# Performance work log

Hardware: AMD Instinct MI355X
Metric: run time of the kernel (lower is better)

The kernel has to match this reference:

```python
import jax, jax.numpy as jnp
import numpy as np

B, NAG = 8192, 16          # scenes, agents per scene
CIN, CH = 64, 128          # gnn_in_channels, gnn_out_channels
R2 = 8.0 * 8.0             # comm_range squared
BOX = 20.0                 # positions sampled uniformly in [0, BOX]^2


def _lin(k, fi, fo):
    k1, k2 = jax.random.split(k)
    s = 1.0 / np.sqrt(fi)
    W = jax.random.uniform(k1, (fi, fo), jnp.float32, -s, s)
    b = jax.random.uniform(k2, (fo,), jnp.float32, -s, s)
    return W, b


def setup_inputs() -> dict:
    key = jax.random.key(0)
    ks = jax.random.split(key, 10)
    x = jax.random.normal(ks[0], (B * NAG, CIN), jnp.float32)          # VAE mu per agent
    pos = jax.random.uniform(ks[1], (B, NAG, 2), jnp.float32) * BOX    # sensor xy positions
    W_rel1, b_rel1 = _lin(ks[2], CIN, CH)
    W_root1, _ = _lin(ks[3], CIN, CH)
    W_rel2, b_rel2 = _lin(ks[4], CH, CH)
    W_root2, _ = _lin(ks[5], CH, CH)
    Wh1, bh1 = _lin(ks[6], 2 * CH, 64)
    Wh2, bh2 = _lin(ks[7], 64, 32)
    Wh3, bh3 = _lin(ks[8], 32, 16)
    return dict(x=x, pos=pos, W_rel1=W_rel1, b_rel1=b_rel1, W_root1=W_root1,
                W_rel2=W_rel2, b_rel2=b_rel2, W_root2=W_root2,
                Wh1=Wh1, bh1=bh1, Wh2=Wh2, bh2=bh2, Wh3=Wh3, bh3=bh3)


def _graph_conv(h, adj, W_rel, b_rel, W_root):
    # PyG GraphConv (aggr='add'): out_i = W_rel @ sum_{j in N(i)} h_j + b_rel + W_root @ h_i
    nb = adj.shape[0]
    hb = h.reshape(nb, NAG, h.shape[-1])                 # [B, n, C]
    agg = jnp.einsum('bij,bjc->bic', adj, hb)            # neighbor sum within each scene
    return agg.reshape(h.shape[0], -1) @ W_rel + b_rel + h @ W_root


def reference(x, pos, W_rel1, b_rel1, W_root1, W_rel2, b_rel2, W_root2,
              Wh1, bh1, Wh2, bh2, Wh3, bh3):
    # radius_graph (batch-isolated, loop=False) as a per-scene dense mask
    diff = pos[:, :, None, :] - pos[:, None, :, :]       # [B, n, n, 2]
    d2 = jnp.sum(diff * diff, axis=-1)                   # [B, n, n]
    eye = jnp.eye(NAG, dtype=bool)
    adj = ((d2 <= R2) & ~eye).astype(x.dtype)            # [B, n, n]
    # Dropout(p=0.2) omitted (eval / deterministic reference).
    x1 = jax.nn.relu(_graph_conv(x, adj, W_rel1, b_rel1, W_root1))   # named 'x1' (inplace ReLU)
    x2 = jax.nn.relu(_graph_conv(x1, adj, W_rel2, b_rel2, W_root2))  # named 'x2' (inplace ReLU)
    h = jnp.concatenate([x1, x2], axis=-1)               # JumpingKnowledge('cat')
    h = jax.nn.relu(h @ Wh1 + bh1)
    h = jax.nn.relu(h @ Wh2 + bh2)
    out = h @ Wh3 + bh3                                  # [N, 16]
    return out.reshape(B, NAG, 16)
```

## Files before the change

kernel.cpp:

```cpp
#include <hip/hip_runtime.h>

#define NSCENE 8192
#define NAG 16
#define R2f 64.0f

typedef unsigned short u16;
typedef __attribute__((ext_vector_type(8))) short short8;
typedef __attribute__((ext_vector_type(4))) float f32x4;

#define OFF_B1 0
#define OFF_B2 16384
#define OFF_H1 49152
#define OFF_H2 65536
#define OFF_H3 67584
#define SWZ_UNITS 8512

__device__ __forceinline__ u16 f2b(float f) {
    unsigned u = __float_as_uint(f);
    unsigned r = u + 0x7FFFu + ((u >> 16) & 1u);
    return (u16)(r >> 16);
}

__global__ __launch_bounds__(256) void swizzle_w(
    const float* __restrict__ Wrel1, const float* __restrict__ Wroot1,
    const float* __restrict__ Wrel2, const float* __restrict__ Wroot2,
    const float* __restrict__ Wh1,  const float* __restrict__ Wh2,
    const float* __restrict__ Wh3,  u16* __restrict__ ws)
{
    const int u = blockIdx.x * 256 + threadIdx.x;
    if (u >= SWZ_UNITS) return;

    int v, T, N, ksplit;
    const float *W, *W2;
    u16* dst;
    if (u < 2048)      { v = u;        T = 8; N = 128; ksplit = 64;  W = Wroot1; W2 = Wrel1; dst = ws + OFF_B1 + v * 8; }
    else if (u < 6144) { v = u - 2048; T = 8; N = 128; ksplit = 128; W = Wroot2; W2 = Wrel2; dst = ws + OFF_B2 + v * 8; }
    else if (u < 8192) { v = u - 6144; T = 4; N = 64;  ksplit = 1 << 30; W = Wh1; W2 = Wh1; dst = ws + OFF_H1 + v * 8; }
    else if (u < 8448) { v = u - 8192; T = 2; N = 32;  ksplit = 1 << 30; W = Wh2; W2 = Wh2; dst = ws + OFF_H2 + v * 8; }
    else               { v = u - 8448; T = 1; N = 16;  ksplit = 1 << 30; W = Wh3; W2 = Wh3; dst = ws + OFF_H3 + v * 8; }

    const int lane = v & 63;
    const int t = (v >> 6) % T;
    const int s = (v >> 6) / T;
    const int n = t * 16 + (lane & 15);
    const int k0 = s * 32 + (lane >> 4) * 8;
    #pragma unroll
    for (int j = 0; j < 8; ++j) {
        const int k = k0 + j;
        const float val = (k < ksplit) ? W[k * N + n] : W2[(k - ksplit) * N + n];
        dst[j] = f2b(val);
    }
}

__device__ __forceinline__ void unpack2(unsigned w, float& a, float& b) {
    a = __uint_as_float(w << 16);
    b = __uint_as_float(w & 0xFFFF0000u);
}

__global__ __launch_bounds__(256) void gnn_mfma(
    const float* __restrict__ x, const float* __restrict__ pos,
    const float* __restrict__ brel1, const float* __restrict__ brel2,
    const float* __restrict__ bh1,  const float* __restrict__ bh2,
    const float* __restrict__ bh3,
    const u16* __restrict__ ws, float* __restrict__ out)
{
    __shared__ __align__(16) u16 XA[16 * 136];
    __shared__ __align__(16) u16 X12[16 * 272];
    __shared__ __align__(16) u16 X2s[16 * 136];
    __shared__ __align__(16) u16 H1s[16 * 72];
    __shared__ __align__(16) u16 H2s[16 * 48];
    __shared__ unsigned mask[NAG];

    const int t = threadIdx.x;
    const int scene = blockIdx.x;
    const int wv = t >> 6;
    const int lane = t & 63;
    const int mrow = lane & 15;
    const int q = lane >> 4;

    {
        const int i0 = t * 4;
        const float4 v = *(const float4*)(x + scene * (NAG * 64) + i0);
        u16* d = &XA[(i0 >> 6) * 136 + (i0 & 63)];
        d[0] = f2b(v.x); d[1] = f2b(v.y); d[2] = f2b(v.z); d[3] = f2b(v.w);
    }
    if (t < NAG) {
        const float* pp = pos + scene * (NAG * 2);
        const float ax = pp[2 * t], ay = pp[2 * t + 1];
        unsigned m = 0;
        for (int j = 0; j < NAG; ++j) {
            const float dx = ax - pp[2 * j], dy = ay - pp[2 * j + 1];
            if (dx * dx + dy * dy <= R2f && j != t) m |= (1u << j);
        }
        mask[t] = m;
    }
    __syncthreads();

    {
        const int a = t >> 4, c0 = (t & 15) * 4;
        const unsigned m = mask[a];
        float s0 = 0.f, s1 = 0.f, s2 = 0.f, s3 = 0.f;
        for (int j = 0; j < NAG; ++j) {
            const unsigned* p = (const unsigned*)&XA[j * 136 + c0];
            float f0, f1, f2, f3;
            unpack2(p[0], f0, f1); unpack2(p[1], f2, f3);
            const bool on = (m >> j) & 1;
            s0 += on ? f0 : 0.f; s1 += on ? f1 : 0.f;
            s2 += on ? f2 : 0.f; s3 += on ? f3 : 0.f;
        }
        u16* d = &XA[a * 136 + 64 + c0];
        d[0] = f2b(s0); d[1] = f2b(s1); d[2] = f2b(s2); d[3] = f2b(s3);
    }
    __syncthreads();

    {
        const float bias0 = brel1[wv * 32 + mrow];
        const float bias1 = brel1[wv * 32 + 16 + mrow];
        f32x4 acc0 = {0.f, 0.f, 0.f, 0.f}, acc1 = acc0;
        #pragma unroll
        for (int s = 0; s < 4; ++s) {
            const short8 a = *(const short8*)&XA[mrow * 136 + s * 32 + q * 8];
            const short8 b0 = *(const short8*)&ws[OFF_B1 + ((s * 8 + 2 * wv) * 64 + lane) * 8];
            const short8 b1 = *(const short8*)&ws[OFF_B1 + ((s * 8 + 2 * wv + 1) * 64 + lane) * 8];
            acc0 = __builtin_amdgcn_mfma_f32_16x16x32_bf16(a, b0, acc0, 0, 0, 0);
            acc1 = __builtin_amdgcn_mfma_f32_16x16x32_bf16(a, b1, acc1, 0, 0, 0);
        }
        #pragma unroll
        for (int r = 0; r < 4; ++r) {
            const int row = q * 4 + r;
            float v0 = acc0[r] + bias0; v0 = v0 > 0.f ? v0 : 0.f;
            float v1 = acc1[r] + bias1; v1 = v1 > 0.f ? v1 : 0.f;
            X12[row * 272 + wv * 32 + mrow] = f2b(v0);
            X12[row * 272 + wv * 32 + 16 + mrow] = f2b(v1);
        }
    }
    __syncthreads();

    {
        const int a = t >> 4, c0 = (t & 15) * 8;
        const unsigned m = mask[a];
        float s0=0.f,s1=0.f,s2=0.f,s3=0.f,s4=0.f,s5=0.f,s6=0.f,s7=0.f;
        for (int j = 0; j < NAG; ++j) {
            const unsigned* p = (const unsigned*)&X12[j * 272 + c0];
            float f0,f1,f2,f3,f4,f5,f6,f7;
            unpack2(p[0], f0, f1); unpack2(p[1], f2, f3);
            unpack2(p[2], f4, f5); unpack2(p[3], f6, f7);
            const bool on = (m >> j) & 1;
            s0 += on ? f0 : 0.f; s1 += on ? f1 : 0.f; s2 += on ? f2 : 0.f; s3 += on ? f3 : 0.f;
            s4 += on ? f4 : 0.f; s5 += on ? f5 : 0.f; s6 += on ? f6 : 0.f; s7 += on ? f7 : 0.f;
        }
        u16* d = &X12[a * 272 + 128 + c0];
        d[0]=f2b(s0); d[1]=f2b(s1); d[2]=f2b(s2); d[3]=f2b(s3);
        d[4]=f2b(s4); d[5]=f2b(s5); d[6]=f2b(s6); d[7]=f2b(s7);
    }
    __syncthreads();

    {
        const float bias0 = brel2[wv * 32 + mrow];
        const float bias1 = brel2[wv * 32 + 16 + mrow];
        f32x4 acc0 = {0.f, 0.f, 0.f, 0.f}, acc1 = acc0;
        #pragma unroll
        for (int s = 0; s < 8; ++s) {
            const short8 a = *(const short8*)&X12[mrow * 272 + s * 32 + q * 8];
            const short8 b0 = *(const short8*)&ws[OFF_B2 + ((s * 8 + 2 * wv) * 64 + lane) * 8];
            const short8 b1 = *(const short8*)&ws[OFF_B2 + ((s * 8 + 2 * wv + 1) * 64 + lane) * 8];
            acc0 = __builtin_amdgcn_mfma_f32_16x16x32_bf16(a, b0, acc0, 0, 0, 0);
            acc1 = __builtin_amdgcn_mfma_f32_16x16x32_bf16(a, b1, acc1, 0, 0, 0);
        }
        #pragma unroll
        for (int r = 0; r < 4; ++r) {
            const int row = q * 4 + r;
            float v0 = acc0[r] + bias0; v0 = v0 > 0.f ? v0 : 0.f;
            float v1 = acc1[r] + bias1; v1 = v1 > 0.f ? v1 : 0.f;
            X2s[row * 136 + wv * 32 + mrow] = f2b(v0);
            X2s[row * 136 + wv * 32 + 16 + mrow] = f2b(v1);
        }
    }
    __syncthreads();

    {
        const float bias = bh1[wv * 16 + mrow];
        f32x4 acc = {0.f, 0.f, 0.f, 0.f};
        #pragma unroll
        for (int s = 0; s < 8; ++s) {
            const short8 a = (s < 4)
                ? *(const short8*)&X12[mrow * 272 + s * 32 + q * 8]
                : *(const short8*)&X2s[mrow * 136 + (s - 4) * 32 + q * 8];
            const short8 b = *(const short8*)&ws[OFF_H1 + ((s * 4 + wv) * 64 + lane) * 8];
            acc = __builtin_amdgcn_mfma_f32_16x16x32_bf16(a, b, acc, 0, 0, 0);
        }
        #pragma unroll
        for (int r = 0; r < 4; ++r) {
            float v = acc[r] + bias; v = v > 0.f ? v : 0.f;
            H1s[(q * 4 + r) * 72 + wv * 16 + mrow] = f2b(v);
        }
    }
    __syncthreads();

    if (wv < 2) {
        const float bias = bh2[wv * 16 + mrow];
        f32x4 acc = {0.f, 0.f, 0.f, 0.f};
        #pragma unroll
        for (int s = 0; s < 2; ++s) {
            const short8 a = *(const short8*)&H1s[mrow * 72 + s * 32 + q * 8];
            const short8 b = *(const short8*)&ws[OFF_H2 + ((s * 2 + wv) * 64 + lane) * 8];
            acc = __builtin_amdgcn_mfma_f32_16x16x32_bf16(a, b, acc, 0, 0, 0);
        }
        #pragma unroll
        for (int r = 0; r < 4; ++r) {
            float v = acc[r] + bias; v = v > 0.f ? v : 0.f;
            H2s[(q * 4 + r) * 48 + wv * 16 + mrow] = f2b(v);
        }
    }
    __syncthreads();

    if (wv == 0) {
        const float bias = bh3[mrow];
        f32x4 acc = {0.f, 0.f, 0.f, 0.f};
        const short8 a = *(const short8*)&H2s[mrow * 48 + q * 8];
        const short8 b = *(const short8*)&ws[OFF_H3 + lane * 8];
        acc = __builtin_amdgcn_mfma_f32_16x16x32_bf16(a, b, acc, 0, 0, 0);
        float* o = out + scene * (NAG * 16);
        #pragma unroll
        for (int r = 0; r < 4; ++r)
            o[(q * 4 + r) * 16 + mrow] = acc[r] + bias;
    }
}

extern "C" void kernel_launch(void* const* d_in, const int* in_sizes, int n_in,
                              void* d_out, int out_size, void* d_ws, size_t ws_size,
                              hipStream_t stream) {
    const float* x      = (const float*)d_in[0];
    const float* pos    = (const float*)d_in[1];
    const float* Wrel1  = (const float*)d_in[2];
    const float* brel1  = (const float*)d_in[3];
    const float* Wroot1 = (const float*)d_in[4];
    const float* Wrel2  = (const float*)d_in[5];
    const float* brel2  = (const float*)d_in[6];
    const float* Wroot2 = (const float*)d_in[7];
    const float* Wh1    = (const float*)d_in[8];
    const float* bh1    = (const float*)d_in[9];
    const float* Wh2    = (const float*)d_in[10];
    const float* bh2    = (const float*)d_in[11];
    const float* Wh3    = (const float*)d_in[12];
    const float* bh3    = (const float*)d_in[13];
    u16* ws = (u16*)d_ws;

    swizzle_w<<<(SWZ_UNITS + 255) / 256, 256, 0, stream>>>(
        Wrel1, Wroot1, Wrel2, Wroot2, Wh1, Wh2, Wh3, ws);
    gnn_mfma<<<NSCENE, 256, 0, stream>>>(
        x, pos, brel1, brel2, bh1, bh2, bh3, ws, (float*)d_out);
}
```

Before: 146.1 us.

## Fuse weight conversion into persistent kernel with register-resident weights and MFMA aggregation

After: 144.2 us. No clear change (-1.3%).

```diff
diff --git a/kernel.cpp b/kernel.cpp
--- a/kernel.cpp
+++ b/kernel.cpp
@@ -1,19 +1,15 @@
 #include <hip/hip_runtime.h>
 
-#define NSCENE 8192
 #define NAG 16
+#define SPB 16
+#define NBLK 512
 #define R2f 64.0f
 
 typedef unsigned short u16;
 typedef __attribute__((ext_vector_type(8))) short short8;
 typedef __attribute__((ext_vector_type(4))) float f32x4;
 
-#define OFF_B1 0
-#define OFF_B2 16384
-#define OFF_H1 49152
-#define OFF_H2 65536
-#define OFF_H3 67584
-#define SWZ_UNITS 8512
+#define MFMA(a, b, c) __builtin_amdgcn_mfma_f32_16x16x32_bf16(a, b, c, 0, 0, 0)
 
 __device__ __forceinline__ u16 f2b(float f) {
     unsigned u = __float_as_uint(f);
@@ -21,209 +17,220 @@
     return (u16)(r >> 16);
 }
 
-__global__ __launch_bounds__(256) void swizzle_w(
-    const float* __restrict__ Wrel1, const float* __restrict__ Wroot1,
-    const float* __restrict__ Wrel2, const float* __restrict__ Wroot2,
-    const float* __restrict__ Wh1,  const float* __restrict__ Wh2,
-    const float* __restrict__ Wh3,  u16* __restrict__ ws)
+__device__ __forceinline__ short8 load_wfrag(const float* __restrict__ W, int N,
+                                             int tile, int s, int q, int mrow) {
+    const float* p = W + (size_t)(s * 32 + q * 8) * N + tile * 16 + mrow;
+    union { short8 v; unsigned u[4]; } r;
+    #pragma unroll
+    for (int jj = 0; jj < 4; ++jj) {
+        const float f0 = p[(2 * jj) * N];
+        const float f1 = p[(2 * jj + 1) * N];
+        r.u[jj] = (unsigned)f2b(f0) | ((unsigned)f2b(f1) << 16);
+    }
+    return r.v;
+}
+
+__device__ __forceinline__ short8 make_adjB(unsigned m, int q) {
+    union { short8 v; unsigned u[4]; } r;
+    #pragma unroll
+    for (int jj = 0; jj < 4; ++jj) {
+        const int k0 = q * 8 + 2 * jj;
+        const unsigned lo = ((m >> k0) & 1u) ? 0x3F80u : 0u;
+        const unsigned hi = ((m >> (k0 + 1)) & 1u) ? 0x3F80u : 0u;
+        r.u[jj] = lo | (hi << 16);
+    }
+    return r.v;
+}
+
+__device__ __forceinline__ void relu_store4(u16* d, f32x4 a) {
+    const unsigned p0 = (unsigned)f2b(fmaxf(a[0], 0.f)) | ((unsigned)f2b(fmaxf(a[1], 0.f)) << 16);
+    const unsigned p1 = (unsigned)f2b(fmaxf(a[2], 0.f)) | ((unsigned)f2b(fmaxf(a[3], 0.f)) << 16);
+    uint2 u; u.x = p0; u.y = p1;
+    *(uint2*)d = u;
+}
+
+__global__ __launch_bounds__(256, 2) void gnn_fused2(
+    const float* __restrict__ x, const float* __restrict__ pos,
+    const float* __restrict__ Wrel1, const float* __restrict__ brel1,
+    const float* __restrict__ Wroot1,
+    const float* __restrict__ Wrel2, const float* __restrict__ brel2,
+    const float* __restrict__ Wroot2,
+    const float* __restrict__ Wh1, const float* __restrict__ bh1,
+    const float* __restrict__ Wh2, const float* __restrict__ bh2,
+    const float* __restrict__ Wh3, const float* __restrict__ bh3,
+    float* __restrict__ out)
 {
-    const int u = blockIdx.x * 256 + threadIdx.x;
-    if (u >= SWZ_UNITS) return;
-
-    int v, T, N, ksplit;
-    const float *W, *W2;
-    u16* dst;
-    if (u < 2048)      { v = u;        T = 8; N = 128; ksplit = 64;  W = Wroot1; W2 = Wrel1; dst = ws + OFF_B1 + v * 8; }
-    else if (u < 6144) { v = u - 2048; T = 8; N = 128; ksplit = 128; W = Wroot2; W2 = Wrel2; dst = ws + OFF_B2 + v * 8; }
-    else if (u < 8192) { v = u - 6144; T = 4; N = 64;  ksplit = 1 << 30; W = Wh1; W2 = Wh1; dst = ws + OFF_H1 + v * 8; }
-    else if (u < 8448) { v = u - 8192; T = 2; N = 32;  ksplit = 1 << 30; W = Wh2; W2 = Wh2; dst = ws + OFF_H2 + v * 8; }
-    else               { v = u - 8448; T = 1; N = 16;  ksplit = 1 << 30; W = Wh3; W2 = Wh3; dst = ws + OFF_H3 + v * 8; }
-
-    const int lane = v & 63;
-    const int t = (v >> 6) % T;
-    const int s = (v >> 6) / T;
-    const int n = t * 16 + (lane & 15);
-    const int k0 = s * 32 + (lane >> 4) * 8;
-    #pragma unroll
-    for (int j = 0; j < 8; ++j) {
-        const int k = k0 + j;
-        const float val = (k < ksplit) ? W[k * N + n] : W2[(k - ksplit) * N + n];
-        dst[j] = f2b(val);
-    }
-}
-
-__device__ __forceinline__ void unpack2(unsigned w, float& a, float& b) {
-    a = __uint_as_float(w << 16);
-    b = __uint_as_float(w & 0xFFFF0000u);
-}
-
-__global__ __launch_bounds__(256) void gnn_mfma(
-    const float* __restrict__ x, const float* __restrict__ pos,
-    const float* __restrict__ brel1, const float* __restrict__ brel2,
-    const float* __restrict__ bh1,  const float* __restrict__ bh2,
-    const float* __restrict__ bh3,
-    const u16* __restrict__ ws, float* __restrict__ out)
-{
-    __shared__ __align__(16) u16 XA[16 * 136];
-    __shared__ __align__(16) u16 X12[16 * 272];
-    __shared__ __align__(16) u16 X2s[16 * 136];
-    __shared__ __align__(16) u16 H1s[16 * 72];
-    __shared__ __align__(16) u16 H2s[16 * 48];
+    __shared__ __align__(16) u16 xb[16 * 72];
+    __shared__ __align__(16) u16 yT[128 * 40];
+    __shared__ __align__(16) u16 x1b[16 * 136];
+    __shared__ __align__(16) u16 x2b[16 * 136];
+    __shared__ __align__(16) u16 h1b[16 * 72];
+    __shared__ __align__(16) u16 h2b[16 * 40];
     __shared__ unsigned mask[NAG];
 
     const int t = threadIdx.x;
-    const int scene = blockIdx.x;
     const int wv = t >> 6;
     const int lane = t & 63;
     const int mrow = lane & 15;
     const int q = lane >> 4;
-
-    {
-        const int i0 = t * 4;
-        const float4 v = *(const float4*)(x + scene * (NAG * 64) + i0);
-        u16* d = &XA[(i0 >> 6) * 136 + (i0 & 63)];
-        d[0] = f2b(v.x); d[1] = f2b(v.y); d[2] = f2b(v.z); d[3] = f2b(v.w);
-    }
-    if (t < NAG) {
-        const float* pp = pos + scene * (NAG * 2);
-        const float ax = pp[2 * t], ay = pp[2 * t + 1];
-        unsigned m = 0;
-        for (int j = 0; j < NAG; ++j) {
-            const float dx = ax - pp[2 * j], dy = ay - pp[2 * j + 1];
-            if (dx * dx + dy * dy <= R2f && j != t) m |= (1u << j);
-        }
-        mask[t] = m;
-    }
-    __syncthreads();
-
-    {
-        const int a = t >> 4, c0 = (t & 15) * 4;
-        const unsigned m = mask[a];
-        float s0 = 0.f, s1 = 0.f, s2 = 0.f, s3 = 0.f;
-        for (int j = 0; j < NAG; ++j) {
-            const unsigned* p = (const unsigned*)&XA[j * 136 + c0];
-            float f0, f1, f2, f3;
-            unpack2(p[0], f0, f1); unpack2(p[1], f2, f3);
-            const bool on = (m >> j) & 1;
-            s0 += on ? f0 : 0.f; s1 += on ? f1 : 0.f;
-            s2 += on ? f2 : 0.f; s3 += on ? f3 : 0.f;
-        }
-        u16* d = &XA[a * 136 + 64 + c0];
-        d[0] = f2b(s0); d[1] = f2b(s1); d[2] = f2b(s2); d[3] = f2b(s3);
-    }
-    __syncthreads();
-
-    {
-        const float bias0 = brel1[wv * 32 + mrow];
-        const float bias1 = brel1[wv * 32 + 16 + mrow];
-        f32x4 acc0 = {0.f, 0.f, 0.f, 0.f}, acc1 = acc0;
+    const int t0 = 2 * wv, t1 = 2 * wv + 1;
+
+    for (int i = t; i < 128 * 16; i += 256)
+        yT[(i >> 4) * 40 + 16 + (i & 15)] = 0;
+
+    short8 wr1[2][2], wo1[2][2], wr2[2][4], wo2[2][4], wh1f[8], wh2f[2], wh3f;
+    #pragma unroll
+    for (int i = 0; i < 2; ++i) {
+        #pragma unroll
+        for (int s = 0; s < 2; ++s) {
+            wr1[i][s] = load_wfrag(Wrel1, 128, t0 + i, s, q, mrow);
+            wo1[i][s] = load_wfrag(Wroot1, 128, t0 + i, s, q, mrow);
+        }
         #pragma unroll
         for (int s = 0; s < 4; ++s) {
-            const short8 a = *(const short8*)&XA[mrow * 136 + s * 32 + q * 8];
-            const short8 b0 = *(const short8*)&ws[OFF_B1 + ((s * 8 + 2 * wv) * 64 + lane) * 8];
-            const short8 b1 = *(const short8*)&ws[OFF_B1 + ((s * 8 + 2 * wv + 1) * 64 + lane) * 8];
-            acc0 = __builtin_amdgcn_mfma_f32_16x16x32_bf16(a, b0, acc0, 0, 0, 0);
-            acc1 = __builtin_amdgcn_mfma_f32_16x16x32_bf16(a, b1, acc1, 0, 0, 0);
-        }
-        #pragma unroll
-        for (int r = 0; r < 4; ++r) {
-            const int row = q * 4 + r;
-            float v0 = acc0[r] + bias0; v0 = v0 > 0.f ? v0 : 0.f;
-            float v1 = acc1[r] + bias1; v1 = v1 > 0.f ? v1 : 0.f;
-            X12[row * 272 + wv * 32 + mrow] = f2b(v0);
-            X12[row * 272 + wv * 32 + 16 + mrow] = f2b(v1);
-        }
-    }
-    __syncthreads();
-
-    {
-        const int a = t >> 4, c0 = (t & 15) * 8;
-        const unsigned m = mask[a];
-        float s0=0.f,s1=0.f,s2=0.f,s3=0.f,s4=0.f,s5=0.f,s6=0.f,s7=0.f;
-        for (int j = 0; j < NAG; ++j) {
-            const unsigned* p = (const unsigned*)&X12[j * 272 + c0];
-            float f0,f1,f2,f3,f4,f5,f6,f7;
-            unpack2(p[0], f0, f1); unpack2(p[1], f2, f3);
-            unpack2(p[2], f4, f5); unpack2(p[3], f6, f7);
-            const bool on = (m >> j) & 1;
-            s0 += on ? f0 : 0.f; s1 += on ? f1 : 0.f; s2 += on ? f2 : 0.f; s3 += on ? f3 : 0.f;
-            s4 += on ? f4 : 0.f; s5 += on ? f5 : 0.f; s6 += on ? f6 : 0.f; s7 += on ? f7 : 0.f;
-        }
-        u16* d = &X12[a * 272 + 128 + c0];
-        d[0]=f2b(s0); d[1]=f2b(s1); d[2]=f2b(s2); d[3]=f2b(s3);
-        d[4]=f2b(s4); d[5]=f2b(s5); d[6]=f2b(s6); d[7]=f2b(s7);
-    }
-    __syncthreads();
-
-    {
-        const float bias0 = brel2[wv * 32 + mrow];
-        const float bias1 = brel2[wv * 32 + 16 + mrow];
-        f32x4 acc0 = {0.f, 0.f, 0.f, 0.f}, acc1 = acc0;
-        #pragma unroll
-        for (int s = 0; s < 8; ++s) {
-            const short8 a = *(const short8*)&X12[mrow * 272 + s * 32 + q * 8];
-            const short8 b0 = *(const short8*)&ws[OFF_B2 + ((s * 8 + 2 * wv) * 64 + lane) * 8];
-            const short8 b1 = *(const short8*)&ws[OFF_B2 + ((s * 8 + 2 * wv + 1) * 64 + lane) * 8];
-            acc0 = __builtin_amdgcn_mfma_f32_16x16x32_bf16(a, b0, acc0, 0, 0, 0);
-            acc1 = __builtin_amdgcn_mfma_f32_16x16x32_bf16(a, b1, acc1, 0, 0, 0);
-        }
-        #pragma unroll
-        for (int r = 0; r < 4; ++r) {
-            const int row = q * 4 + r;
-            float v0 = acc0[r] + bias0; v0 = v0 > 0.f ? v0 : 0.f;
-            float v1 = acc1[r] + bias1; v1 = v1 > 0.f ? v1 : 0.f;
-            X2s[row * 136 + wv * 32 + mrow] = f2b(v0);
-            X2s[row * 136 + wv * 32 + 16 + mrow] = f2b(v1);
-        }
-    }
-    __syncthreads();
-
-    {
-        const float bias = bh1[wv * 16 + mrow];
-        f32x4 acc = {0.f, 0.f, 0.f, 0.f};
-        #pragma unroll
-        for (int s = 0; s < 8; ++s) {
-            const short8 a = (s < 4)
-                ? *(const short8*)&X12[mrow * 272 + s * 32 + q * 8]
-                : *(const short8*)&X2s[mrow * 136 + (s - 4) * 32 + q * 8];
-            const short8 b = *(const short8*)&ws[OFF_H1 + ((s * 4 + wv) * 64 + lane) * 8];
-            acc = __builtin_amdgcn_mfma_f32_16x16x32_bf16(a, b, acc, 0, 0, 0);
-        }
-        #pragma unroll
-        for (int r = 0; r < 4; ++r) {
-            float v = acc[r] + bias; v = v > 0.f ? v : 0.f;
-            H1s[(q * 4 + r) * 72 + wv * 16 + mrow] = f2b(v);
-        }
-    }
-    __syncthreads();
-
-    if (wv < 2) {
-        const float bias = bh2[wv * 16 + mrow];
-        f32x4 acc = {0.f, 0.f, 0.f, 0.f};
-        #pragma unroll
-        for (int s = 0; s < 2; ++s) {
-            const short8 a = *(const short8*)&H1s[mrow * 72 + s * 32 + q * 8];
-            const short8 b = *(const short8*)&ws[OFF_H2 + ((s * 2 + wv) * 64 + lane) * 8];
-            acc = __builtin_amdgcn_mfma_f32_16x16x32_bf16(a, b, acc, 0, 0, 0);
-        }
-        #pragma unroll
-        for (int r = 0; r < 4; ++r) {
-            float v = acc[r] + bias; v = v > 0.f ? v : 0.f;
-            H2s[(q * 4 + r) * 48 + wv * 16 + mrow] = f2b(v);
-        }
-    }
-    __syncthreads();
-
-    if (wv == 0) {
-        const float bias = bh3[mrow];
-        f32x4 acc = {0.f, 0.f, 0.f, 0.f};
-        const short8 a = *(const short8*)&H2s[mrow * 48 + q * 8];
-        const short8 b = *(const short8*)&ws[OFF_H3 + lane * 8];
-        acc = __builtin_amdgcn_mfma_f32_16x16x32_bf16(a, b, acc, 0, 0, 0);
-        float* o = out + scene * (NAG * 16);
-        #pragma unroll
-        for (int r = 0; r < 4; ++r)
-            o[(q * 4 + r) * 16 + mrow] = acc[r] + bias;
+            wr2[i][s] = load_wfrag(Wrel2, 128, t0 + i, s, q, mrow);
+            wo2[i][s] = load_wfrag(Wroot2, 128, t0 + i, s, q, mrow);
+        }
+    }
+    #pragma unroll
+    for (int s = 0; s < 8; ++s) wh1f[s] = load_wfrag(Wh1, 64, wv, s, q, mrow);
+    #pragma unroll
+    for (int s = 0; s < 2; ++s) wh2f[s] = load_wfrag(Wh2, 32, wv & 1, s, q, mrow);
+    wh3f = load_wfrag(Wh3, 16, 0, 0, q, mrow);
+
+    const float4 br1a = *(const float4*)(brel1 + t0 * 16 + q * 4);
+    const float4 br1b = *(const float4*)(brel1 + t1 * 16 + q * 4);
+    const float4 br2a = *(const float4*)(brel2 + t0 * 16 + q * 4);
+    const float4 br2b = *(const float4*)(brel2 + t1 * 16 + q * 4);
+    const float4 bb1  = *(const float4*)(bh1 + wv * 16 + q * 4);
+    const float4 bb2  = *(const float4*)(bh2 + (wv & 1) * 16 + q * 4);
+    const float4 bb3  = *(const float4*)(bh3 + q * 4);
+
+    #pragma unroll 1
+    for (int g = 0; g < SPB; ++g) {
+        const size_t scene = (size_t)blockIdx.x * SPB + g;
+
+        {
+            const int i0 = t * 4;
+            const float4 v = *(const float4*)(x + scene * (NAG * 64) + i0);
+            const unsigned p0 = (unsigned)f2b(v.x) | ((unsigned)f2b(v.y) << 16);
+            const unsigned p1 = (unsigned)f2b(v.z) | ((unsigned)f2b(v.w) << 16);
+            uint2 u; u.x = p0; u.y = p1;
+            *(uint2*)&xb[(i0 >> 6) * 72 + (i0 & 63)] = u;
+        }
+        if (t < NAG) {
+            const float* pp = pos + scene * (NAG * 2);
+            const float ax = pp[2 * t], ay = pp[2 * t + 1];
+            unsigned m = 0;
+            for (int j = 0; j < NAG; ++j) {
+                const float dx = ax - pp[2 * j], dy = ay - pp[2 * j + 1];
+                if (dx * dx + dy * dy <= R2f && j != t) m |= (1u << j);
+            }
+            mask[t] = m;
+        }
+        __syncthreads();
+
+        const short8 adjB = make_adjB(mask[mrow], q);
+
+        {
+            f32x4 a0 = {0.f, 0.f, 0.f, 0.f}, a1 = a0;
+            #pragma unroll
+            for (int s = 0; s < 2; ++s) {
+                const short8 b = *(const short8*)&xb[mrow * 72 + s * 32 + q * 8];
+                a0 = MFMA(wr1[0][s], b, a0);
+                a1 = MFMA(wr1[1][s], b, a1);
+            }
+            #pragma unroll
+            for (int r = 0; r < 4; ++r) {
+                yT[(t0 * 16 + q * 4 + r) * 40 + mrow] = f2b(a0[r]);
+                yT[(t1 * 16 + q * 4 + r) * 40 + mrow] = f2b(a1[r]);
+            }
+        }
+        __syncthreads();
+
+        {
+            f32x4 a0 = {br1a.x, br1a.y, br1a.z, br1a.w};
+            f32x4 a1 = {br1b.x, br1b.y, br1b.z, br1b.w};
+            const short8 ya0 = *(const short8*)&yT[(t0 * 16 + mrow) * 40 + q * 8];
+            const short8 ya1 = *(const short8*)&yT[(t1 * 16 + mrow) * 40 + q * 8];
+            a0 = MFMA(ya0, adjB, a0);
+            a1 = MFMA(ya1, adjB, a1);
+            #pragma unroll
+            for (int s = 0; s < 2; ++s) {
+                const short8 b = *(const short8*)&xb[mrow * 72 + s * 32 + q * 8];
+                a0 = MFMA(wo1[0][s], b, a0);
+                a1 = MFMA(wo1[1][s], b, a1);
+            }
+            relu_store4(&x1b[mrow * 136 + t0 * 16 + q * 4], a0);
+            relu_store4(&x1b[mrow * 136 + t1 * 16 + q * 4], a1);
+        }
+        __syncthreads();
+
+        {
+            f32x4 a0 = {0.f, 0.f, 0.f, 0.f}, a1 = a0;
+            #pragma unroll
+            for (int s = 0; s < 4; ++s) {
+                const short8 b = *(const short8*)&x1b[mrow * 136 + s * 32 + q * 8];
+                a0 = MFMA(wr2[0][s], b, a0);
+                a1 = MFMA(wr2[1][s], b, a1);
+            }
+            #pragma unroll
+            for (int r = 0; r < 4; ++r) {
+                yT[(t0 * 16 + q * 4 + r) * 40 + mrow] = f2b(a0[r]);
+                yT[(t1 * 16 + q * 4 + r) * 40 + mrow] = f2b(a1[r]);
+            }
+        }
+        __syncthreads();
+
+        {
+            f32x4 a0 = {br2a.x, br2a.y, br2a.z, br2a.w};
+            f32x4 a1 = {br2b.x, br2b.y, br2b.z, br2b.w};
+            const short8 ya0 = *(const short8*)&yT[(t0 * 16 + mrow) * 40 + q * 8];
+            const short8 ya1 = *(const short8*)&yT[(t1 * 16 + mrow) * 40 + q * 8];
+            a0 = MFMA(ya0, adjB, a0);
+            a1 = MFMA(ya1, adjB, a1);
+            #pragma unroll
+            for (int s = 0; s < 4; ++s) {
+                const short8 b = *(const short8*)&x1b[mrow * 136 + s * 32 + q * 8];
+                a0 = MFMA(wo2[0][s], b, a0);
+                a1 = MFMA(wo2[1][s], b, a1);
+            }
+            relu_store4(&x2b[mrow * 136 + t0 * 16 + q * 4], a0);
+            relu_store4(&x2b[mrow * 136 + t1 * 16 + q * 4], a1);
+        }
+        __syncthreads();
+
+        {
+            f32x4 a = {bb1.x, bb1.y, bb1.z, bb1.w};
+            #pragma unroll
+            for (int s = 0; s < 8; ++s) {
+                const short8 b = (s < 4)
+                    ? *(const short8*)&x1b[mrow * 136 + s * 32 + q * 8]
+                    : *(const short8*)&x2b[mrow * 136 + (s - 4) * 32 + q * 8];
+                a = MFMA(wh1f[s], b, a);
+            }
+            relu_store4(&h1b[mrow * 72 + wv * 16 + q * 4], a);
+        }
+        __syncthreads();
+
+        if (wv < 2) {
+            f32x4 a = {bb2.x, bb2.y, bb2.z, bb2.w};
+            #pragma unroll
+            for (int s = 0; s < 2; ++s) {
+                const short8 b = *(const short8*)&h1b[mrow * 72 + s * 32 + q * 8];
+                a = MFMA(wh2f[s], b, a);
+            }
+            relu_store4(&h2b[mrow * 40 + wv * 16 + q * 4], a);
+        }
+        __syncthreads();
+
+        if (wv == 0) {
+            f32x4 a = {bb3.x, bb3.y, bb3.z, bb3.w};
+            const short8 b = *(const short8*)&h2b[mrow * 40 + q * 8];
+            a = MFMA(wh3f, b, a);
+            float4 o; o.x = a[0]; o.y = a[1]; o.z = a[2]; o.w = a[3];
+            *(float4*)(out + scene * (NAG * 16) + mrow * 16 + q * 4) = o;
+        }
     }
 }
 
@@ -244,10 +251,8 @@
     const float* bh2    = (const float*)d_in[11];
     const float* Wh3    = (const float*)d_in[12];
     const float* bh3    = (const float*)d_in[13];
-    u16* ws = (u16*)d_ws;
-
-    swizzle_w<<<(SWZ_UNITS + 255) / 256, 256, 0, stream>>>(
-        Wrel1, Wroot1, Wrel2, Wroot2, Wh1, Wh2, Wh3, ws);
-    gnn_mfma<<<NSCENE, 256, 0, stream>>>(
-        x, pos, brel1, brel2, bh1, bh2, bh3, ws, (float*)d_out);
-}
+
+    gnn_fused2<<<NBLK, 256, 0, stream>>>(
+        x, pos, Wrel1, brel1, Wroot1, Wrel2, brel2, Wroot2,
+        Wh1, bh1, Wh2, bh2, Wh3, bh3, (float*)d_out);
+}
```

## Batch two scenes per pass, 4 per block, and do neighbor aggregation via MFMA

Applied to the files above, without the earlier changes.

New measurement: 166.4 us. +13.9%, slower.

```diff
diff --git a/kernel.cpp b/kernel.cpp
--- a/kernel.cpp
+++ b/kernel.cpp
@@ -1,12 +1,15 @@
 #include <hip/hip_runtime.h>
 
-#define NSCENE 8192
 #define NAG 16
+#define SPB 4
+#define NBLK 2048
 #define R2f 64.0f
 
 typedef unsigned short u16;
 typedef __attribute__((ext_vector_type(8))) short short8;
 typedef __attribute__((ext_vector_type(4))) float f32x4;
+
+#define MFMA(a, b, c) __builtin_amdgcn_mfma_f32_16x16x32_bf16(a, b, c, 0, 0, 0)
 
 #define OFF_B1 0
 #define OFF_B2 16384
@@ -52,178 +55,228 @@
     }
 }
 
-__device__ __forceinline__ void unpack2(unsigned w, float& a, float& b) {
-    a = __uint_as_float(w << 16);
-    b = __uint_as_float(w & 0xFFFF0000u);
-}
-
-__global__ __launch_bounds__(256) void gnn_mfma(
+__device__ __forceinline__ short8 ldfrag(const u16* __restrict__ ws, int off,
+                                         int T, int s, int tile, int lane) {
+    return *(const short8*)(ws + off + (size_t)(((s * T + tile) * 64 + lane) * 8));
+}
+
+__device__ __forceinline__ short8 make_adjB(unsigned m, int q) {
+    union { short8 v; unsigned u[4]; } r;
+    #pragma unroll
+    for (int jj = 0; jj < 4; ++jj) {
+        const int k0 = q * 8 + 2 * jj;
+        const unsigned lo = ((m >> k0) & 1u) ? 0x3F80u : 0u;
+        const unsigned hi = ((m >> (k0 + 1)) & 1u) ? 0x3F80u : 0u;
+        r.u[jj] = lo | (hi << 16);
+    }
+    return r.v;
+}
+
+__device__ __forceinline__ void relu_store4(u16* d, f32x4 a) {
+    const unsigned p0 = (unsigned)f2b(fmaxf(a[0], 0.f)) | ((unsigned)f2b(fmaxf(a[1], 0.f)) << 16);
+    const unsigned p1 = (unsigned)f2b(fmaxf(a[2], 0.f)) | ((unsigned)f2b(fmaxf(a[3], 0.f)) << 16);
+    uint2 u; u.x = p0; u.y = p1;
+    *(uint2*)d = u;
+}
+
+__global__ __launch_bounds__(256) void gnn_fused3(
     const float* __restrict__ x, const float* __restrict__ pos,
     const float* __restrict__ brel1, const float* __restrict__ brel2,
     const float* __restrict__ bh1,  const float* __restrict__ bh2,
     const float* __restrict__ bh3,
     const u16* __restrict__ ws, float* __restrict__ out)
 {
-    __shared__ __align__(16) u16 XA[16 * 136];
-    __shared__ __align__(16) u16 X12[16 * 272];
-    __shared__ __align__(16) u16 X2s[16 * 136];
-    __shared__ __align__(16) u16 H1s[16 * 72];
-    __shared__ __align__(16) u16 H2s[16 * 48];
-    __shared__ unsigned mask[NAG];
+    __shared__ __align__(16) u16 xb[2][16 * 72];
+    __shared__ __align__(16) u16 yT[2][128 * 40];
+    __shared__ __align__(16) u16 x1b[2][16 * 136];
+    __shared__ __align__(16) u16 x2b[2][16 * 136];
+    __shared__ __align__(16) u16 h1b[2][16 * 72];
+    __shared__ __align__(16) u16 h2b[2][16 * 40];
+    __shared__ unsigned mask[2][NAG];
 
     const int t = threadIdx.x;
-    const int scene = blockIdx.x;
-    const int wv = t >> 6;
-    const int lane = t & 63;
-    const int mrow = lane & 15;
-    const int q = lane >> 4;
-
-    {
-        const int i0 = t * 4;
-        const float4 v = *(const float4*)(x + scene * (NAG * 64) + i0);
-        u16* d = &XA[(i0 >> 6) * 136 + (i0 & 63)];
-        d[0] = f2b(v.x); d[1] = f2b(v.y); d[2] = f2b(v.z); d[3] = f2b(v.w);
+    const int wv = t >> 6, lane = t & 63, mrow = lane & 15, q = lane >> 4;
+    const int t0 = 2 * wv, t1 = 2 * wv + 1;
+
+    for (int i = t; i < 2 * 128 * 16; i += 256) {
+        const int slot = i >> 11, rem = i & 2047;
+        yT[slot][(rem >> 4) * 40 + 16 + (rem & 15)] = 0;
     }
-    if (t < NAG) {
-        const float* pp = pos + scene * (NAG * 2);
-        const float ax = pp[2 * t], ay = pp[2 * t + 1];
-        unsigned m = 0;
-        for (int j = 0; j < NAG; ++j) {
-            const float dx = ax - pp[2 * j], dy = ay - pp[2 * j + 1];
-            if (dx * dx + dy * dy <= R2f && j != t) m |= (1u << j);
-        }
-        mask[t] = m;
-    }
-    __syncthreads();
-
-    {
-        const int a = t >> 4, c0 = (t & 15) * 4;
-        const unsigned m = mask[a];
-        float s0 = 0.f, s1 = 0.f, s2 = 0.f, s3 = 0.f;
-        for (int j = 0; j < NAG; ++j) {
-            const unsigned* p = (const unsigned*)&XA[j * 136 + c0];
-            float f0, f1, f2, f3;
-            unpack2(p[0], f0, f1); unpack2(p[1], f2, f3);
-            const bool on = (m >> j) & 1;
-            s0 += on ? f0 : 0.f; s1 += on ? f1 : 0.f;
-            s2 += on ? f2 : 0.f; s3 += on ? f3 : 0.f;
-        }
-        u16* d = &XA[a * 136 + 64 + c0];
-        d[0] = f2b(s0); d[1] = f2b(s1); d[2] = f2b(s2); d[3] = f2b(s3);
-    }
-    __syncthreads();
-
-    {
-        const float bias0 = brel1[wv * 32 + mrow];
-        const float bias1 = brel1[wv * 32 + 16 + mrow];
-        f32x4 acc0 = {0.f, 0.f, 0.f, 0.f}, acc1 = acc0;
-        #pragma unroll
-        for (int s = 0; s < 4; ++s) {
-            const short8 a = *(const short8*)&XA[mrow * 136 + s * 32 + q * 8];
-            const short8 b0 = *(const short8*)&ws[OFF_B1 + ((s * 8 + 2 * wv) * 64 + lane) * 8];
-            const short8 b1 = *(const short8*)&ws[OFF_B1 + ((s * 8 + 2 * wv + 1) * 64 + lane) * 8];
-            acc0 = __builtin_amdgcn_mfma_f32_16x16x32_bf16(a, b0, acc0, 0, 0, 0);
-            acc1 = __builtin_amdgcn_mfma_f32_16x16x32_bf16(a, b1, acc1, 0, 0, 0);
-        }
-        #pragma unroll
-        for (int r = 0; r < 4; ++r) {
-            const int row = q * 4 + r;
-            float v0 = acc0[r] + bias0; v0 = v0 > 0.f ? v0 : 0.f;
-            float v1 = acc1[r] + bias1; v1 = v1 > 0.f ? v1 : 0.f;
-            X12[row * 272 + wv * 32 + mrow] = f2b(v0);
-            X12[row * 272 + wv * 32 + 16 + mrow] = f2b(v1);
-        }
-    }
-    __syncthreads();
-
-    {
-        const int a = t >> 4, c0 = (t & 15) * 8;
-        const unsigned m = mask[a];
-        float s0=0.f,s1=0.f,s2=0.f,s3=0.f,s4=0.f,s5=0.f,s6=0.f,s7=0.f;
-        for (int j = 0; j < NAG; ++j) {
-            const unsigned* p = (const unsigned*)&X12[j * 272 + c0];
-            float f0,f1,f2,f3,f4,f5,f6,f7;
-            unpack2(p[0], f0, f1); unpack2(p[1], f2, f3);
-            unpack2(p[2], f4, f5); unpack2(p[3], f6, f7);
-            const bool on = (m >> j) & 1;
-            s0 += on ? f0 : 0.f; s1 += on ? f1 : 0.f; s2 += on ? f2 : 0.f; s3 += on ? f3 : 0.f;
-            s4 += on ? f4 : 0.f; s5 += on ? f5 : 0.f; s6 += on ? f6 : 0.f; s7 += on ? f7 : 0.f;
-        }
-        u16* d = &X12[a * 272 + 128 + c0];
-        d[0]=f2b(s0); d[1]=f2b(s1); d[2]=f2b(s2); d[3]=f2b(s3);
-        d[4]=f2b(s4); d[5]=f2b(s5); d[6]=f2b(s6); d[7]=f2b(s7);
-    }
-    __syncthreads();
-
-    {
-        const float bias0 = brel2[wv * 32 + mrow];
-        const float bias1 = brel2[wv * 32 + 16 + mrow];
-        f32x4 acc0 = {0.f, 0.f, 0.f, 0.f}, acc1 = acc0;
-        #pragma unroll
-        for (int s = 0; s < 8; ++s) {
-            const short8 a = *(const short8*)&X12[mrow * 272 + s * 32 + q * 8];
-            const short8 b0 = *(const short8*)&ws[OFF_B2 + ((s * 8 + 2 * wv) * 64 + lane) * 8];
-            const short8 b1 = *(const short8*)&ws[OFF_B2 + ((s * 8 + 2 * wv + 1) * 64 + lane) * 8];
-            acc0 = __builtin_amdgcn_mfma_f32_16x16x32_bf16(a, b0, acc0, 0, 0, 0);
-            acc1 = __builtin_amdgcn_mfma_f32_16x16x32_bf16(a, b1, acc1, 0, 0, 0);
-        }
-        #pragma unroll
-        for (int r = 0; r < 4; ++r) {
-            const int row = q * 4 + r;
-            float v0 = acc0[r] + bias0; v0 = v0 > 0.f ? v0 : 0.f;
-            float v1 = acc1[r] + bias1; v1 = v1 > 0.f ? v1 : 0.f;
-            X2s[row * 136 + wv * 32 + mrow] = f2b(v0);
-            X2s[row * 136 + wv * 32 + 16 + mrow] = f2b(v1);
-        }
-    }
-    __syncthreads();
-
-    {
-        const float bias = bh1[wv * 16 + mrow];
-        f32x4 acc = {0.f, 0.f, 0.f, 0.f};
-        #pragma unroll
-        for (int s = 0; s < 8; ++s) {
-            const short8 a = (s < 4)
-                ? *(const short8*)&X12[mrow * 272 + s * 32 + q * 8]
-                : *(const short8*)&X2s[mrow * 136 + (s - 4) * 32 + q * 8];
-            const short8 b = *(const short8*)&ws[OFF_H1 + ((s * 4 + wv) * 64 + lane) * 8];
-            acc = __builtin_amdgcn_mfma_f32_16x16x32_bf16(a, b, acc, 0, 0, 0);
-        }
-        #pragma unroll
-        for (int r = 0; r < 4; ++r) {
-            float v = acc[r] + bias; v = v > 0.f ? v : 0.f;
-            H1s[(q * 4 + r) * 72 + wv * 16 + mrow] = f2b(v);
-        }
-    }
-    __syncthreads();
-
-    if (wv < 2) {
-        const float bias = bh2[wv * 16 + mrow];
-        f32x4 acc = {0.f, 0.f, 0.f, 0.f};
-        #pragma unroll
-        for (int s = 0; s < 2; ++s) {
-            const short8 a = *(const short8*)&H1s[mrow * 72 + s * 32 + q * 8];
-            const short8 b = *(const short8*)&ws[OFF_H2 + ((s * 2 + wv) * 64 + lane) * 8];
-            acc = __builtin_amdgcn_mfma_f32_16x16x32_bf16(a, b, acc, 0, 0, 0);
-        }
-        #pragma unroll
-        for (int r = 0; r < 4; ++r) {
-            float v = acc[r] + bias; v = v > 0.f ? v : 0.f;
-            H2s[(q * 4 + r) * 48 + wv * 16 + mrow] = f2b(v);
-        }
-    }
-    __syncthreads();
-
-    if (wv == 0) {
-        const float bias = bh3[mrow];
-        f32x4 acc = {0.f, 0.f, 0.f, 0.f};
-        const short8 a = *(const short8*)&H2s[mrow * 48 + q * 8];
-        const short8 b = *(const short8*)&ws[OFF_H3 + lane * 8];
-        acc = __builtin_amdgcn_mfma_f32_16x16x32_bf16(a, b, acc, 0, 0, 0);
-        float* o = out + scene * (NAG * 16);
-        #pragma unroll
-        for (int r = 0; r < 4; ++r)
-            o[(q * 4 + r) * 16 + mrow] = acc[r] + bias;
+
+    const float4 br1a = *(const float4*)(brel1 + t0 * 16 + q * 4);
+    const float4 br1b = *(const float4*)(brel1 + t1 * 16 + q * 4);
+    const float4 br2a = *(const float4*)(brel2 + t0 * 16 + q * 4);
+    const float4 br2b = *(const float4*)(brel2 + t1 * 16 + q * 4);
+    const float4 bb1  = *(const float4*)(bh1 + wv * 16 + q * 4);
+    const float4 bb2  = *(const float4*)(bh2 + (wv & 1) * 16 + q * 4);
+    const float4 bb3  = *(const float4*)(bh3 + q * 4);
+
+    #pragma unroll 1
+    for (int g = 0; g < SPB / 2; ++g) {
+        const size_t sA = (size_t)blockIdx.x * SPB + 2 * g;
+
+        {
+            const int i0 = t * 4;
+            #pragma unroll
+            for (int sl = 0; sl < 2; ++sl) {
+                const float4 v = *(const float4*)(x + (sA + sl) * (NAG * 64) + i0);
+                const unsigned p0 = (unsigned)f2b(v.x) | ((unsigned)f2b(v.y) << 16);
+                const unsigned p1 = (unsigned)f2b(v.z) | ((unsigned)f2b(v.w) << 16);
+                uint2 u; u.x = p0; u.y = p1;
+                *(uint2*)&xb[sl][(i0 >> 6) * 72 + (i0 & 63)] = u;
+            }
+        }
+        if (t < 32) {
+            const int sl = t >> 4, a = t & 15;
+            const float* pp = pos + (sA + sl) * (NAG * 2);
+            const float ax = pp[2 * a], ay = pp[2 * a + 1];
+            unsigned m = 0;
+            for (int j = 0; j < NAG; ++j) {
+                const float dx = ax - pp[2 * j], dy = ay - pp[2 * j + 1];
+                if (dx * dx + dy * dy <= R2f && j != a) m |= (1u << j);
+            }
+            mask[sl][a] = m;
+        }
+        __syncthreads();
+
+        const short8 adjA = make_adjB(mask[0][mrow], q);
+        const short8 adjBv = make_adjB(mask[1][mrow], q);
+
+        {
+            f32x4 aA0 = {0.f,0.f,0.f,0.f}, aA1 = aA0, aB0 = aA0, aB1 = aA0;
+            #pragma unroll
+            for (int s = 0; s < 2; ++s) {
+                const short8 w0 = ldfrag(ws, OFF_B1, 8, s + 2, t0, lane);
+                const short8 w1 = ldfrag(ws, OFF_B1, 8, s + 2, t1, lane);
+                const short8 bA = *(const short8*)&xb[0][mrow * 72 + s * 32 + q * 8];
+                const short8 bB = *(const short8*)&xb[1][mrow * 72 + s * 32 + q * 8];
+                aA0 = MFMA(w0, bA, aA0); aA1 = MFMA(w1, bA, aA1);
+                aB0 = MFMA(w0, bB, aB0); aB1 = MFMA(w1, bB, aB1);
+            }
+            #pragma unroll
+            for (int r = 0; r < 4; ++r) {
+                yT[0][(t0 * 16 + q * 4 + r) * 40 + mrow] = f2b(aA0[r]);
+                yT[0][(t1 * 16 + q * 4 + r) * 40 + mrow] = f2b(aA1[r]);
+                yT[1][(t0 * 16 + q * 4 + r) * 40 + mrow] = f2b(aB0[r]);
+                yT[1][(t1 * 16 + q * 4 + r) * 40 + mrow] = f2b(aB1[r]);
+            }
+        }
+        __syncthreads();
+
+        {
+            f32x4 aA0 = {br1a.x, br1a.y, br1a.z, br1a.w};
+            f32x4 aA1 = {br1b.x, br1b.y, br1b.z, br1b.w};
+            f32x4 aB0 = aA0, aB1 = aA1;
+            const short8 yA0 = *(const short8*)&yT[0][(t0 * 16 + mrow) * 40 + q * 8];
+            const short8 yA1 = *(const short8*)&yT[0][(t1 * 16 + mrow) * 40 + q * 8];
+            const short8 yB0 = *(const short8*)&yT[1][(t0 * 16 + mrow) * 40 + q * 8];
+            const short8 yB1 = *(const short8*)&yT[1][(t1 * 16 + mrow) * 40 + q * 8];
+            aA0 = MFMA(yA0, adjA, aA0);  aA1 = MFMA(yA1, adjA, aA1);
+            aB0 = MFMA(yB0, adjBv, aB0); aB1 = MFMA(yB1, adjBv, aB1);
+            #pragma unroll
+            for (int s = 0; s < 2; ++s) {
+                const short8 w0 = ldfrag(ws, OFF_B1, 8, s, t0, lane);
+                const short8 w1 = ldfrag(ws, OFF_B1, 8, s, t1, lane);
+                const short8 bA = *(const short8*)&xb[0][mrow * 72 + s * 32 + q * 8];
+                const short8 bB = *(const short8*)&xb[1][mrow * 72 + s * 32 + q * 8];
+                aA0 = MFMA(w0, bA, aA0); aA1 = MFMA(w1, bA, aA1);
+                aB0 = MFMA(w0, bB, aB0); aB1 = MFMA(w1, bB, aB1);
+            }
+            relu_store4(&x1b[0][mrow * 136 + t0 * 16 + q * 4], aA0);
+            relu_store4(&x1b[0][mrow * 136 + t1 * 16 + q * 4], aA1);
+            relu_store4(&x1b[1][mrow * 136 + t0 * 16 + q * 4], aB0);
+            relu_store4(&x1b[1][mrow * 136 + t1 * 16 + q * 4], aB1);
+        }
+        __syncthreads();
+
+        {
+            f32x4 aA0 = {0.f,0.f,0.f,0.f}, aA1 = aA0, aB0 = aA0, aB1 = aA0;
+            #pragma unroll
+            for (int s = 0; s < 4; ++s) {
+                const short8 w0 = ldfrag(ws, OFF_B2, 8, s + 4, t0, lane);
+                const short8 w1 = ldfrag(ws, OFF_B2, 8, s + 4, t1, lane);
+                const short8 bA = *(const short8*)&x1b[0][mrow * 136 + s * 32 + q * 8];
+                const short8 bB = *(const short8*)&x1b[1][mrow * 136 + s * 32 + q * 8];
+                aA0 = MFMA(w0, bA, aA0); aA1 = MFMA(w1, bA, aA1);
+                aB0 = MFMA(w0, bB, aB0); aB1 = MFMA(w1, bB, aB1);
+            }
+            #pragma unroll
+            for (int r = 0; r < 4; ++r) {
+                yT[0][(t0 * 16 + q * 4 + r) * 40 + mrow] = f2b(aA0[r]);
+                yT[0][(t1 * 16 + q * 4 + r) * 40 + mrow] = f2b(aA1[r]);
+                yT[1][(t0 * 16 + q * 4 + r) * 40 + mrow] = f2b(aB0[r]);
+                yT[1][(t1 * 16 + q * 4 + r) * 40 + mrow] = f2b(aB1[r]);
+            }
+        }
+        __syncthreads();
+
+        {
+            f32x4 aA0 = {br2a.x, br2a.y, br2a.z, br2a.w};
+            f32x4 aA1 = {br2b.x, br2b.y, br2b.z, br2b.w};
+            f32x4 aB0 = aA0, aB1 = aA1;
+            const short8 yA0 = *(const short8*)&yT[0][(t0 * 16 + mrow) * 40 + q * 8];
+            const short8 yA1 = *(const short8*)&yT[0][(t1 * 16 + mrow) * 40 + q * 8];
+            const short8 yB0 = *(const short8*)&yT[1][(t0 * 16 + mrow) * 40 + q * 8];
+            const short8 yB1 = *(const short8*)&yT[1][(t1 * 16 + mrow) * 40 + q * 8];
+            aA0 = MFMA(yA0, adjA, aA0);  aA1 = MFMA(yA1, adjA, aA1);
+            aB0 = MFMA(yB0, adjBv, aB0); aB1 = MFMA(yB1, adjBv, aB1);
+            #pragma unroll
+            for (int s = 0; s < 4; ++s) {
+                const short8 w0 = ldfrag(ws, OFF_B2, 8, s, t0, lane);
+                const short8 w1 = ldfrag(ws, OFF_B2, 8, s, t1, lane);
+                const short8 bA = *(const short8*)&x1b[0][mrow * 136 + s * 32 + q * 8];
+                const short8 bB = *(const short8*)&x1b[1][mrow * 136 + s * 32 + q * 8];
+                aA0 = MFMA(w0, bA, aA0); aA1 = MFMA(w1, bA, aA1);
+                aB0 = MFMA(w0, bB, aB0); aB1 = MFMA(w1, bB, aB1);
+            }
+            relu_store4(&x2b[0][mrow * 136 + t0 * 16 + q * 4], aA0);
+            relu_store4(&x2b[0][mrow * 136 + t1 * 16 + q * 4], aA1);
+            relu_store4(&x2b[1][mrow * 136 + t0 * 16 + q * 4], aB0);
+            relu_store4(&x2b[1][mrow * 136 + t1 * 16 + q * 4], aB1);
+        }
+        __syncthreads();
+
+        {
+            f32x4 aA = {bb1.x, bb1.y, bb1.z, bb1.w};
+            f32x4 aB = aA;
+            #pragma unroll
+            for (int s = 0; s < 8; ++s) {
+                const short8 w = ldfrag(ws, OFF_H1, 4, s, wv, lane);
+                const short8 bA = (s < 4)
+                    ? *(const short8*)&x1b[0][mrow * 136 + s * 32 + q * 8]
+                    : *(const short8*)&x2b[0][mrow * 136 + (s - 4) * 32 + q * 8];
+                const short8 bB = (s < 4)
+                    ? *(const short8*)&x1b[1][mrow * 136 + s * 32 + q * 8]
+                    : *(const short8*)&x2b[1][mrow * 136 + (s - 4) * 32 + q * 8];
+                aA = MFMA(w, bA, aA);
+                aB = MFMA(w, bB, aB);
+            }
+            relu_store4(&h1b[0][mrow * 72 + wv * 16 + q * 4], aA);
+            relu_store4(&h1b[1][mrow * 72 + wv * 16 + q * 4], aB);
+        }
+        __syncthreads();
+
+        {
+            const int slot = wv >> 1, tile = wv & 1;
+            f32x4 a = {bb2.x, bb2.y, bb2.z, bb2.w};
+            #pragma unroll
+            for (int s = 0; s < 2; ++s) {
+                const short8 w = ldfrag(ws, OFF_H2, 2, s, tile, lane);
+                const short8 b = *(const short8*)&h1b[slot][mrow * 72 + s * 32 + q * 8];
+                a = MFMA(w, b, a);
+            }
+            relu_store4(&h2b[slot][mrow * 40 + tile * 16 + q * 4], a);
+        }
+        __syncthreads();
+
+        if (wv < 2) {
+            f32x4 a = {bb3.x, bb3.y, bb3.z, bb3.w};
+            const short8 w = ldfrag(ws, OFF_H3, 1, 0, 0, lane);
+            const short8 b = *(const short8*)&h2b[wv][mrow * 40 + q * 8];
+            a = MFMA(w, b, a);
+            float4 o; o.x = a[0]; o.y = a[1]; o.z = a[2]; o.w = a[3];
+            *(float4*)(out + (sA + wv) * (NAG * 16) + mrow * 16 + q * 4) = o;
+        }
     }
 }
 
@@ -248,6 +301,6 @@
 
     swizzle_w<<<(SWZ_UNITS + 255) / 256, 256, 0, stream>>>(
         Wrel1, Wroot1, Wrel2, Wroot2, Wh1, Wh2, Wh3, ws);
-    gnn_mfma<<<NSCENE, 256, 0, stream>>>(
+    gnn_fused3<<<NBLK, 256, 0, stream>>>(
         x, pos, brel1, brel2, bh1, bh2, bh3, ws, (float*)d_out);
 }
```
